# Optimization experiments

Measured on AMD Instinct MI355X. Metric: run time of the kernel, lower is better.

The kernel has to match this reference:

```python
import jax, jax.numpy as jnp
import numpy as np


def _attention(v, W, static_hidden, dec_hidden):
    # static_hidden: [B,N,H], dec_hidden: [B,1,H], v: [1,1,H], W: [1,H,2H]
    hidden = jnp.concatenate(
        [static_hidden, jnp.broadcast_to(dec_hidden, static_hidden.shape)], axis=2
    )  # [B,N,2H]
    e = jnp.tanh(jnp.einsum('bnk,hk->bnh', hidden, W[0]))  # W @ hidden^T, done row-wise
    scores = jnp.einsum('bnh,h->bn', e, v[0, 0])  # [B,N]
    return jax.nn.softmax(scores, axis=1)[:, None, :]  # [B,1,N]


def _gru_step(x, h, w_ih, w_hh, b_ih, b_hh):
    # x: [B,H] input, h: [B,H] prev hidden; PyTorch gate order: r | z | n
    gx = x @ w_ih.T + b_ih  # [B,3H]
    gh = h @ w_hh.T + b_hh  # [B,3H]
    H = h.shape[-1]
    r = jax.nn.sigmoid(gx[:, :H] + gh[:, :H])
    z = jax.nn.sigmoid(gx[:, H:2 * H] + gh[:, H:2 * H])
    n = jnp.tanh(gx[:, 2 * H:] + r * gh[:, 2 * H:])
    return (1.0 - z) * n + z * h


def _pointer_scores(v, W, static_hidden, context, state_embedding):
    # energy = cat(static, context, state_emb) -> [B,N,3H]
    energy = jnp.concatenate(
        [static_hidden,
         jnp.broadcast_to(context, static_hidden.shape),
         jnp.broadcast_to(state_embedding, static_hidden.shape)], axis=2)
    e = jnp.tanh(jnp.einsum('bnk,hk->bnh', energy, W[0]))  # [B,N,H]
    return jnp.einsum('bnh,h->bn', e, v[0, 0])  # [B,N]


def setup_inputs() -> dict:
    key = jax.random.key(0)
    B, N, H = 128, 512, 512
    ks = jax.random.split(key, 16)
    s = 0.05
    return {
        'static_hidden': jax.random.normal(ks[0], (B, N, H), jnp.float32),
        'state_embedding': jax.random.normal(ks[1], (B, 1, H), jnp.float32),
        'decoder_hidden': jax.random.normal(ks[2], (B, 1, H), jnp.float32),
        'target_hidden': jax.random.normal(ks[3], (B, 1, H), jnp.float32),
        'last_hh': jax.random.normal(ks[4], (1, B, H), jnp.float32),
        # Pointer params (note: target branch of the original reuses self.v/self.W)
        'ptr_v': jax.random.normal(ks[5], (1, 1, H), jnp.float32) * s,
        'ptr_W': jax.random.normal(ks[6], (1, H, 3 * H), jnp.float32) * s,
        # encoder attention params
        'enc_v': jax.random.normal(ks[7], (1, 1, H), jnp.float32) * s,
        'enc_W': jax.random.normal(ks[8], (1, H, 2 * H), jnp.float32) * s,
        # target attention params
        'tgt_v': jax.random.normal(ks[9], (1, 1, H), jnp.float32) * s,
        'tgt_W': jax.random.normal(ks[10], (1, H, 2 * H), jnp.float32) * s,
        # GRU (single layer) params
        'gru_w_ih': jax.random.normal(ks[11], (3 * H, H), jnp.float32) * s,
        'gru_w_hh': jax.random.normal(ks[12], (3 * H, H), jnp.float32) * s,
        'gru_b_ih': jax.random.normal(ks[13], (3 * H,), jnp.float32) * s,
        'gru_b_hh': jax.random.normal(ks[14], (3 * H,), jnp.float32) * s,
    }


def reference(static_hidden, state_embedding, decoder_hidden, target_hidden, last_hh,
              ptr_v, ptr_W, enc_v, enc_W, tgt_v, tgt_W,
              gru_w_ih, gru_w_hh, gru_b_ih, gru_b_hh):
    # GRU over seq len 1 (batch_first); dropout layers are identity (eval mode)
    h_new = _gru_step(decoder_hidden[:, 0, :], last_hh[0], gru_w_ih, gru_w_hh, gru_b_ih, gru_b_hh)
    rnn_out = h_new[:, None, :]          # [B,1,H]
    new_last_hh = h_new[None]            # [1,B,H]

    # encoder attention + context
    enc_attn = _attention(enc_v, enc_W, static_hidden, rnn_out)   # [B,1,N]
    context = jnp.matmul(enc_attn, static_hidden)                 # [B,1,H]
    probs = _pointer_scores(ptr_v, ptr_W, static_hidden, context, state_embedding)

    # target attention + context (original reuses self.v/self.W for scoring)
    tgt_attn = _attention(tgt_v, tgt_W, static_hidden, target_hidden)
    context_t = jnp.matmul(tgt_attn, static_hidden)
    probs_target = _pointer_scores(ptr_v, ptr_W, static_hidden, context_t, state_embedding)

    probs = 5.0 * probs + probs_target
    return (probs, new_last_hh)
```

## Files before the change

### kernel.cpp

```cpp
#include <hip/hip_runtime.h>
#include <math.h>

#define B 128
#define N 512
#define H 512

typedef __attribute__((ext_vector_type(8))) short short8;
typedef __attribute__((ext_vector_type(4))) float floatx4;

__device__ __forceinline__ float sigmoidf_(float x){ return 1.0f/(1.0f+__expf(-x)); }

__device__ __forceinline__ float fast_tanh(float x){
    float t = __expf(-2.0f*fabsf(x));
    float r = __fdividef(1.0f - t, 1.0f + t);
    return copysignf(r, x);
}

__device__ __forceinline__ unsigned f2bf1(float f){
    unsigned u = __float_as_uint(f);
    u += 0x7FFFu + ((u>>16)&1u);
    return u>>16;
}
__device__ __forceinline__ unsigned pk2(float a, float b){
    return f2bf1(a) | (f2bf1(b)<<16);
}

__global__ __launch_bounds__(256) void k_castA(const float* __restrict__ A,
    unsigned short* __restrict__ Abf)
{
    size_t i = ((size_t)blockIdx.x*256 + threadIdx.x)*8;
    float4 lo = *(const float4*)&A[i];
    float4 hi = *(const float4*)&A[i+4];
    uint4 p;
    p.x = pk2(lo.x,lo.y); p.y = pk2(lo.z,lo.w);
    p.z = pk2(hi.x,hi.y); p.w = pk2(hi.z,hi.w);
    *(uint4*)&Abf[i] = p;
}

__global__ __launch_bounds__(256) void k_castw(
    const float* __restrict__ encW, const float* __restrict__ tgtW,
    const float* __restrict__ ptrW, const float* __restrict__ wih,
    const float* __restrict__ whh,
    unsigned short* __restrict__ We_s, unsigned short* __restrict__ Wt_s,
    unsigned short* __restrict__ Wp_s, unsigned short* __restrict__ We_d,
    unsigned short* __restrict__ Wt_d, unsigned short* __restrict__ Wp_c,
    unsigned short* __restrict__ Wp_e, unsigned short* __restrict__ Wih_b,
    unsigned short* __restrict__ Whh_b)
{
    int r = blockIdx.x, t = threadIdx.x;
    const float* src; unsigned short* dst; int pitch, off, row;
    if (r < 512)      { src=encW; dst=We_s; pitch=2*H; off=0;   row=r; }
    else if (r<1024)  { src=tgtW; dst=Wt_s; pitch=2*H; off=0;   row=r-512; }
    else if (r<1536)  { src=ptrW; dst=Wp_s; pitch=3*H; off=0;   row=r-1024; }
    else if (r<2048)  { src=encW; dst=We_d; pitch=2*H; off=H;   row=r-1536; }
    else if (r<2560)  { src=tgtW; dst=Wt_d; pitch=2*H; off=H;   row=r-2048; }
    else if (r<3072)  { src=ptrW; dst=Wp_c; pitch=3*H; off=H;   row=r-2560; }
    else if (r<3584)  { src=ptrW; dst=Wp_e; pitch=3*H; off=2*H; row=r-3072; }
    else if (r<5120)  { src=wih;  dst=Wih_b;pitch=H;   off=0;   row=r-3584; }
    else              { src=whh;  dst=Whh_b;pitch=H;   off=0;   row=r-5120; }
    float2 v = *(const float2*)&src[(size_t)row*pitch + off + 2*t];
    *(unsigned*)&dst[(size_t)row*H + 2*t] = pk2(v.x, v.y);
}

__global__ __launch_bounds__(256) void k_castX(const float* __restrict__ dec,
    const float* __restrict__ lhh, const float* __restrict__ tgt,
    const float* __restrict__ sem,
    unsigned short* __restrict__ Xbf, unsigned short* __restrict__ Hbf,
    unsigned short* __restrict__ Tbf, unsigned short* __restrict__ Sbf)
{
    int blk = blockIdx.x; int mat = blk >> 5;
    const float* src = mat==0?dec : mat==1?lhh : mat==2?tgt : sem;
    unsigned short* dst = mat==0?Xbf : mat==1?Hbf : mat==2?Tbf : Sbf;
    size_t i = ((size_t)(blk&31)*256 + threadIdx.x)*8;
    float4 lo = *(const float4*)&src[i];
    float4 hi = *(const float4*)&src[i+4];
    uint4 p;
    p.x = pk2(lo.x,lo.y); p.y = pk2(lo.z,lo.w);
    p.z = pk2(hi.x,hi.y); p.w = pk2(hi.z,hi.w);
    *(uint4*)&dst[i] = p;
}

__global__ __launch_bounds__(256) void k_castctx(const float* __restrict__ ctx,
    const float* __restrict__ ctxt,
    unsigned short* __restrict__ CXbf, unsigned short* __restrict__ CTbf)
{
    int blk = blockIdx.x; int mat = blk >> 5;
    const float* src = mat ? ctxt : ctx;
    unsigned short* dst = mat ? CTbf : CXbf;
    size_t i = ((size_t)(blk&31)*256 + threadIdx.x)*8;
    float4 lo = *(const float4*)&src[i];
    float4 hi = *(const float4*)&src[i+4];
    uint4 p;
    p.x = pk2(lo.x,lo.y); p.y = pk2(lo.z,lo.w);
    p.z = pk2(hi.x,hi.y); p.w = pk2(hi.z,hi.w);
    *(uint4*)&dst[i] = p;
}

__device__ __forceinline__ void gemm128_tile(
    const unsigned short* __restrict__ Ab,
    const unsigned short* __restrict__ Bb,
    float* __restrict__ C, int ldc)
{
    __shared__ __align__(16) unsigned short As[128*64];
    __shared__ __align__(16) unsigned short Bs[128*64];
    int t = threadIdx.x;
    int lane = t & 63, wave = t >> 6;
    int wy = wave >> 1, wx = wave & 1;
    int li = lane & 15, quad = lane >> 4;

    floatx4 acc[4][4];
    #pragma unroll
    for (int i=0;i<4;++i)
      #pragma unroll
      for (int j=0;j<4;++j) acc[i][j] = (floatx4)(0.0f);

    for (int kt=0; kt<8; ++kt){
        int k0 = kt*64;
        #pragma unroll
        for (int c=0;c<4;++c){
            int idx = c*256 + t;
            int row = idx >> 3, kb = idx & 7;
            uint4 va = *(const uint4*)&Ab[(size_t)row*512 + k0 + kb*8];
            *(uint4*)&As[row*64 + ((kb ^ (row&7))*8)] = va;
            uint4 vb = *(const uint4*)&Bb[(size_t)row*512 + k0 + kb*8];
            *(uint4*)&Bs[row*64 + ((kb ^ (row&7))*8)] = vb;
        }
        __syncthreads();
        #pragma unroll
        for (int ks=0;ks<2;++ks){
            short8 af[4], bg[4];
            #pragma unroll
            for (int i=0;i<4;++i){
                int m = wy*64 + i*16 + li;
                int kb = (ks*4 + quad) ^ (m&7);
                af[i] = *(const short8*)&As[m*64 + kb*8];
            }
            #pragma unroll
            for (int j=0;j<4;++j){
                int h = wx*64 + j*16 + li;
                int kb = (ks*4 + quad) ^ (h&7);
                bg[j] = *(const short8*)&Bs[h*64 + kb*8];
            }
            #pragma unroll
            for (int i=0;i<4;++i)
              #pragma unroll
              for (int j=0;j<4;++j)
                acc[i][j] = __builtin_amdgcn_mfma_f32_16x16x32_bf16(af[i], bg[j], acc[i][j], 0,0,0);
        }
        __syncthreads();
    }
    #pragma unroll
    for (int i=0;i<4;++i)
      #pragma unroll
      for (int j=0;j<4;++j)
        #pragma unroll
        for (int rg=0;rg<4;++rg){
            int m = wy*64 + i*16 + quad*4 + rg;
            int n = wx*64 + j*16 + li;
            C[(size_t)m*ldc + n] = acc[i][j][rg];
        }
}

__global__ __launch_bounds__(256,2) void k_gru_gemm(
    const unsigned short* __restrict__ Xbf, const unsigned short* __restrict__ Hbf,
    const unsigned short* __restrict__ Wih_b, const unsigned short* __restrict__ Whh_b,
    float* __restrict__ gx, float* __restrict__ gh)
{
    int blk = blockIdx.x;
    int mat = blk / 12, nt = blk % 12;
    const unsigned short* Ab = mat ? Hbf : Xbf;
    const unsigned short* Bb = (mat ? Whh_b : Wih_b) + (size_t)nt*128*512;
    float* C = (mat ? gh : gx) + nt*128;
    gemm128_tile(Ab, Bb, C, 3*H);
}

__global__ __launch_bounds__(256) void k_gru_gate(const float* __restrict__ gx,
    const float* __restrict__ gh, const float* __restrict__ lhh,
    const float* __restrict__ bih, const float* __restrict__ bhh,
    float* __restrict__ out_hh, unsigned short* __restrict__ hnew_bf)
{
    int idx = blockIdx.x*256 + threadIdx.x;
    int b = idx >> 9, k = idx & 511;
    const float* gxb = gx + (size_t)b*(3*H);
    const float* ghb = gh + (size_t)b*(3*H);
    float r = sigmoidf_(gxb[k]     + bih[k]     + ghb[k]     + bhh[k]);
    float z = sigmoidf_(gxb[H+k]   + bih[H+k]   + ghb[H+k]   + bhh[H+k]);
    float n = tanhf(gxb[2*H+k] + bih[2*H+k] + r*(ghb[2*H+k] + bhh[2*H+k]));
    float h = (1.f-z)*n + z*lhh[idx];
    out_hh[idx] = h;
    hnew_bf[idx] = (unsigned short)f2bf1(h);
}

__global__ __launch_bounds__(256,2) void k_bias_gemm(
    const unsigned short* __restrict__ HNbf, const unsigned short* __restrict__ Tbf,
    const unsigned short* __restrict__ Sbf,
    const unsigned short* __restrict__ We_d, const unsigned short* __restrict__ Wt_d,
    const unsigned short* __restrict__ Wp_e,
    float* __restrict__ d_enc, float* __restrict__ d_tgt, float* __restrict__ d_se)
{
    int blk = blockIdx.x;
    int mat = blk >> 2, nt = blk & 3;
    const unsigned short* Ab = mat==0 ? HNbf : mat==1 ? Tbf : Sbf;
    const unsigned short* Bb = (mat==0 ? We_d : mat==1 ? Wt_d : Wp_e) + (size_t)nt*128*512;
    float* C = (mat==0 ? d_enc : mat==1 ? d_tgt : d_se) + nt*128;
    gemm128_tile(Ab, Bb, C, H);
}

__global__ __launch_bounds__(256,2) void k_dptr_gemm(
    const unsigned short* __restrict__ CXbf, const unsigned short* __restrict__ CTbf,
    const unsigned short* __restrict__ Wp_c,
    float* __restrict__ d_pe, float* __restrict__ d_pt)
{
    int blk = blockIdx.x;
    int mat = blk >> 2, nt = blk & 3;
    const unsigned short* Ab = mat ? CTbf : CXbf;
    const unsigned short* Bb = Wp_c + (size_t)nt*128*512;
    float* C = (mat ? d_pt : d_pe) + nt*128;
    gemm128_tile(Ab, Bb, C, H);
}

template<bool BF16A>
__global__ __launch_bounds__(256,2) void k_scores_fused(
    const float* __restrict__ Af, const unsigned short* __restrict__ Abf,
    const unsigned short* __restrict__ We, const unsigned short* __restrict__ Wt,
    const float* __restrict__ d_enc, const float* __restrict__ d_tgt,
    const float* __restrict__ enc_v, const float* __restrict__ tgt_v,
    float* __restrict__ sc_e, float* __restrict__ sc_t)
{
    __shared__ __align__(16) unsigned short As[128*64];
    __shared__ __align__(16) unsigned short Be[128*64];
    __shared__ __align__(16) unsigned short Bt[128*64];
    int blk = blockIdx.x;
    int b = blk >> 4; int nt = (blk >> 2) & 3; int ht = blk & 3;
    int n0 = nt*128, hb = ht*128;
    int t = threadIdx.x;
    int lane = t & 63, wave = t >> 6;
    int wy = wave >> 1, wx = wave & 1;
    int li = lane & 15, quad = lane >> 4;

    floatx4 acc_e[4][4], acc_t[4][4];
    #pragma unroll
    for (int i=0;i<4;++i)
      #pragma unroll
      for (int j=0;j<4;++j){ acc_e[i][j]=(floatx4)(0.0f); acc_t[i][j]=(floatx4)(0.0f); }

    for (int kt=0; kt<8; ++kt){
        int k0 = kt*64;
        #pragma unroll
        for (int c=0;c<4;++c){
            int idx = c*256 + t;
            int row = idx >> 3, kb = idx & 7;
            if constexpr (BF16A){
                uint4 v = *(const uint4*)&Abf[(size_t)(b*N+n0+row)*H + k0 + kb*8];
                *(uint4*)&As[row*64 + ((kb ^ (row&7))*8)] = v;
            } else {
                const float* src = Af + (size_t)(b*N+n0+row)*H + k0 + kb*8;
                float4 lo = *(const float4*)src;
                float4 hi = *(const float4*)(src+4);
                uint4 p;
                p.x = pk2(lo.x,lo.y); p.y = pk2(lo.z,lo.w);
                p.z = pk2(hi.x,hi.y); p.w = pk2(hi.z,hi.w);
                *(uint4*)&As[row*64 + ((kb ^ (row&7))*8)] = p;
            }
        }
        #pragma unroll
        for (int c=0;c<4;++c){
            int idx = c*256 + t;
            int row = idx >> 3, kb = idx & 7;
            uint4 v = *(const uint4*)&We[(size_t)(hb+row)*H + k0 + kb*8];
            *(uint4*)&Be[row*64 + ((kb ^ (row&7))*8)] = v;
            uint4 w = *(const uint4*)&Wt[(size_t)(hb+row)*H + k0 + kb*8];
            *(uint4*)&Bt[row*64 + ((kb ^ (row&7))*8)] = w;
        }
        __syncthreads();
        #pragma unroll
        for (int ks=0;ks<2;++ks){
            short8 af[4], be[4], bt[4];
            #pragma unroll
            for (int i=0;i<4;++i){
                int m = wy*64 + i*16 + li;
                int kb = (ks*4 + quad) ^ (m&7);
                af[i] = *(const short8*)&As[m*64 + kb*8];
            }
            #pragma unroll
            for (int j=0;j<4;++j){
                int h = wx*64 + j*16 + li;
                int kb = (ks*4 + quad) ^ (h&7);
                be[j] = *(const short8*)&Be[h*64 + kb*8];
                bt[j] = *(const short8*)&Bt[h*64 + kb*8];
            }
            #pragma unroll
            for (int i=0;i<4;++i)
              #pragma unroll
              for (int j=0;j<4;++j){
                acc_e[i][j] = __builtin_amdgcn_mfma_f32_16x16x32_bf16(af[i], be[j], acc_e[i][j], 0,0,0);
                acc_t[i][j] = __builtin_amdgcn_mfma_f32_16x16x32_bf16(af[i], bt[j], acc_t[i][j], 0,0,0);
              }
        }
        __syncthreads();
    }
    float nse[4][4], nst[4][4];
    #pragma unroll
    for (int i=0;i<4;++i)
      #pragma unroll
      for (int rg=0;rg<4;++rg){ nse[i][rg]=0.f; nst[i][rg]=0.f; }
    #pragma unroll
    for (int j=0;j<4;++j){
        int hm = hb + wx*64 + j*16 + li;
        float dje = d_enc[b*H+hm], vje = enc_v[hm];
        float djt = d_tgt[b*H+hm], vjt = tgt_v[hm];
        #pragma unroll
        for (int i=0;i<4;++i)
          #pragma unroll
          for (int rg=0;rg<4;++rg){
            nse[i][rg] += vje * fast_tanh(acc_e[i][j][rg] + dje);
            nst[i][rg] += vjt * fast_tanh(acc_t[i][j][rg] + djt);
          }
    }
    #pragma unroll
    for (int off=1; off<16; off<<=1)
      #pragma unroll
      for (int i=0;i<4;++i)
        #pragma unroll
        for (int rg=0;rg<4;++rg){
          nse[i][rg] += __shfl_xor(nse[i][rg], off);
          nst[i][rg] += __shfl_xor(nst[i][rg], off);
        }
    if (li==0){
        #pragma unroll
        for (int i=0;i<4;++i)
          #pragma unroll
          for (int rg=0;rg<4;++rg){
            atomicAdd(&sc_e[b*N + n0 + wy*64 + i*16 + quad*4 + rg], nse[i][rg]);
            atomicAdd(&sc_t[b*N + n0 + wy*64 + i*16 + quad*4 + rg], nst[i][rg]);
          }
    }
}

__global__ __launch_bounds__(256) void k_softmax(const float* __restrict__ sc_e,
    const float* __restrict__ sc_t, float* __restrict__ w_e, float* __restrict__ w_t)
{
    __shared__ float buf[256];
    int b = blockIdx.x, t = threadIdx.x;
    float x0 = sc_e[b*N+t], x1 = sc_e[b*N+t+256];
    float m = fmaxf(x0,x1);
    buf[t]=m; __syncthreads();
    for (int s2=128;s2>0;s2>>=1){ if(t<s2) buf[t]=fmaxf(buf[t],buf[t+s2]); __syncthreads(); }
    m = buf[0]; __syncthreads();
    float e0 = __expf(x0-m), e1 = __expf(x1-m);
    buf[t]=e0+e1; __syncthreads();
    for (int s2=128;s2>0;s2>>=1){ if(t<s2) buf[t]+=buf[t+s2]; __syncthreads(); }
    float inv = 1.0f/buf[0]; __syncthreads();
    w_e[b*N+t]=e0*inv; w_e[b*N+t+256]=e1*inv;
    x0 = sc_t[b*N+t]; x1 = sc_t[b*N+t+256];
    m = fmaxf(x0,x1);
    buf[t]=m; __syncthreads();
    for (int s2=128;s2>0;s2>>=1){ if(t<s2) buf[t]=fmaxf(buf[t],buf[t+s2]); __syncthreads(); }
    m = buf[0]; __syncthreads();
    e0 = __expf(x0-m); e1 = __expf(x1-m);
    buf[t]=e0+e1; __syncthreads();
    for (int s2=128;s2>0;s2>>=1){ if(t<s2) buf[t]+=buf[t+s2]; __syncthreads(); }
    inv = 1.0f/buf[0];
    w_t[b*N+t]=e0*inv; w_t[b*N+t+256]=e1*inv;
}

__global__ __launch_bounds__(256) void k_context_bf16(const unsigned short* __restrict__ Abf,
    const float* __restrict__ w_e, const float* __restrict__ w_t,
    float* __restrict__ ctx, float* __restrict__ ctxt)
{
    __shared__ float we[64], wt[64];
    int b = blockIdx.x >> 3, c = blockIdx.x & 7, t = threadIdx.x;
    int n0 = c*64;
    if (t < 64){ we[t]=w_e[b*N+n0+t]; wt[t]=w_t[b*N+n0+t]; }
    __syncthreads();
    float ae0=0.f, ae1=0.f, at0=0.f, at1=0.f;
    for (int n=0;n<64;++n){
        unsigned u = *(const unsigned*)&Abf[(size_t)(b*N+n0+n)*H + 2*t];
        float lo = __uint_as_float(u<<16);
        float hi = __uint_as_float(u & 0xFFFF0000u);
        float e = we[n], g = wt[n];
        ae0 += e*lo; ae1 += e*hi; at0 += g*lo; at1 += g*hi;
    }
    atomicAdd(&ctx[b*H+2*t],   ae0); atomicAdd(&ctx[b*H+2*t+1],  ae1);
    atomicAdd(&ctxt[b*H+2*t],  at0); atomicAdd(&ctxt[b*H+2*t+1], at1);
}

__global__ __launch_bounds__(256) void k_context(const float* __restrict__ A,
    const float* __restrict__ w_e, const float* __restrict__ w_t,
    float* __restrict__ ctx, float* __restrict__ ctxt)
{
    __shared__ float we[128], wt[128];
    int b = blockIdx.x >> 2, c = blockIdx.x & 3, t = threadIdx.x;
    int n0 = c*128;
    if (t < 128){ we[t]=w_e[b*N+n0+t]; wt[t]=w_t[b*N+n0+t]; }
    __syncthreads();
    float ae0=0.f, ae1=0.f, at0=0.f, at1=0.f;
    for (int n=0;n<128;++n){
        const float* ar = A + (size_t)(b*N + n0 + n)*H;
        float a0 = ar[t], a1 = ar[t+256];
        ae0 += we[n]*a0; ae1 += we[n]*a1;
        at0 += wt[n]*a0; at1 += wt[n]*a1;
    }
    atomicAdd(&ctx[b*H+t],      ae0); atomicAdd(&ctx[b*H+t+256],  ae1);
    atomicAdd(&ctxt[b*H+t],     at0); atomicAdd(&ctxt[b*H+t+256], at1);
}

template<bool BF16A>
__global__ __launch_bounds__(256) void k_probs_mfma(
    const float* __restrict__ Af, const unsigned short* __restrict__ Abf,
    const unsigned short* __restrict__ Wp,
    const float* __restrict__ d_pe, const float* __restrict__ d_pt,
    const float* __restrict__ d_se,
    const float* __restrict__ ptr_v, float* __restrict__ probs)
{
    __shared__ __align__(16) unsigned short As[128*64];
    __shared__ __align__(16) unsigned short Bs[128*64];
    int blk = blockIdx.x;
    int b = blk >> 4; int nt = (blk >> 2) & 3; int ht = blk & 3;
    int n0 = nt*128, hb = ht*128;

    int t = threadIdx.x;
    int lane = t & 63, wave = t >> 6;
    int wy = wave >> 1, wx = wave & 1;
    int li = lane & 15, quad = lane >> 4;

    floatx4 acc[4][4];
    #pragma unroll
    for (int i=0;i<4;++i)
      #pragma unroll
      for (int j=0;j<4;++j) acc[i][j] = (floatx4)(0.0f);

    for (int kt=0; kt<8; ++kt){
        int k0 = kt*64;
        #pragma unroll
        for (int c=0;c<4;++c){
            int idx = c*256 + t;
            int row = idx >> 3, kb = idx & 7;
            if constexpr (BF16A){
                uint4 v = *(const uint4*)&Abf[(size_t)(b*N+n0+row)*H + k0 + kb*8];
                *(uint4*)&As[row*64 + ((kb ^ (row&7))*8)] = v;
            } else {
                const float* src = Af + (size_t)(b*N+n0+row)*H + k0 + kb*8;
                float4 lo = *(const float4*)src;
                float4 hi = *(const float4*)(src+4);
                uint4 p;
                p.x = pk2(lo.x,lo.y); p.y = pk2(lo.z,lo.w);
                p.z = pk2(hi.x,hi.y); p.w = pk2(hi.z,hi.w);
                *(uint4*)&As[row*64 + ((kb ^ (row&7))*8)] = p;
            }
        }
        #pragma unroll
        for (int c=0;c<4;++c){
            int idx = c*256 + t;
            int row = idx >> 3, kb = idx & 7;
            uint4 v = *(const uint4*)&Wp[(size_t)(hb+row)*H + k0 + kb*8];
            *(uint4*)&Bs[row*64 + ((kb ^ (row&7))*8)] = v;
        }
        __syncthreads();
        #pragma unroll
        for (int ks=0;ks<2;++ks){
            short8 af[4], bg[4];
            #pragma unroll
            for (int i=0;i<4;++i){
                int m = wy*64 + i*16 + li;
                int kb = (ks*4 + quad) ^ (m&7);
                af[i] = *(const short8*)&As[m*64 + kb*8];
            }
            #pragma unroll
            for (int j=0;j<4;++j){
                int h = wx*64 + j*16 + li;
                int kb = (ks*4 + quad) ^ (h&7);
                bg[j] = *(const short8*)&Bs[h*64 + kb*8];
            }
            #pragma unroll
            for (int i=0;i<4;++i)
              #pragma unroll
              for (int j=0;j<4;++j)
                acc[i][j] = __builtin_amdgcn_mfma_f32_16x16x32_bf16(af[i], bg[j], acc[i][j], 0,0,0);
        }
        __syncthreads();
    }
    float nsum[4][4];
    #pragma unroll
    for (int i=0;i<4;++i){ nsum[i][0]=0.f;nsum[i][1]=0.f;nsum[i][2]=0.f;nsum[i][3]=0.f; }
    #pragma unroll
    for (int j=0;j<4;++j){
        int hm = hb + wx*64 + j*16 + li;
        float se = d_se[b*H + hm];
        float de = d_pe[b*H + hm] + se;
        float dt = d_pt[b*H + hm] + se;
        float vj = ptr_v[hm];
        #pragma unroll
        for (int i=0;i<4;++i)
          #pragma unroll
          for (int rg=0;rg<4;++rg){
            float s = acc[i][j][rg];
            nsum[i][rg] += vj * (5.0f*fast_tanh(s + de) + fast_tanh(s + dt));
          }
    }
    #pragma unroll
    for (int off=1; off<16; off<<=1)
      #pragma unroll
      for (int i=0;i<4;++i)
        #pragma unroll
        for (int rg=0;rg<4;++rg)
          nsum[i][rg] += __shfl_xor(nsum[i][rg], off);
    if (li==0){
        #pragma unroll
        for (int i=0;i<4;++i)
          #pragma unroll
          for (int rg=0;rg<4;++rg)
            atomicAdd(&probs[b*N + n0 + wy*64 + i*16 + quad*4 + rg], nsum[i][rg]);
    }
}

extern "C" void kernel_launch(void* const* d_in, const int* in_sizes, int n_in,
                              void* d_out, int out_size, void* d_ws, size_t ws_size,
                              hipStream_t stream)
{
    (void)in_sizes; (void)n_in; (void)out_size;
    const float* A    = (const float*)d_in[0];
    const float* sem  = (const float*)d_in[1];
    const float* dec  = (const float*)d_in[2];
    const float* tgt  = (const float*)d_in[3];
    const float* lhh  = (const float*)d_in[4];
    const float* ptrv = (const float*)d_in[5];
    const float* ptrW = (const float*)d_in[6];
    const float* encv = (const float*)d_in[7];
    const float* encW = (const float*)d_in[8];
    const float* tgtv = (const float*)d_in[9];
    const float* tgtW = (const float*)d_in[10];
    const float* wih  = (const float*)d_in[11];
    const float* whh  = (const float*)d_in[12];
    const float* bih  = (const float*)d_in[13];
    const float* bhh  = (const float*)d_in[14];

    float* probs_out = (float*)d_out;
    float* hh_out    = (float*)d_out + B*N;

    float* ws = (float*)d_ws;
    const size_t S = (size_t)B*H;
    float* d_enc = ws;
    float* d_tgt = ws + S;
    float* d_se  = ws + 2*S;
    float* sc_e  = ws + 3*S;
    float* sc_t  = ws + 4*S;
    float* ctx   = ws + 5*S;
    float* ctxt  = ws + 6*S;
    float* w_e   = ws + 7*S;
    float* w_t   = ws + 8*S;
    float* d_pe  = ws + 9*S;
    float* d_pt  = ws + 10*S;
    float* gx    = ws + 11*S;
    float* gh    = ws + 14*S;
    unsigned short* bfb  = (unsigned short*)(ws + 17*S);
    const size_t WH = (size_t)H*H;
    const size_t WG = (size_t)3*H*H;
    unsigned short* We_s  = bfb;
    unsigned short* Wt_s  = We_s + WH;
    unsigned short* Wp_s  = Wt_s + WH;
    unsigned short* We_d  = Wp_s + WH;
    unsigned short* Wt_d  = We_d + WH;
    unsigned short* Wp_c  = Wt_d + WH;
    unsigned short* Wp_e  = Wp_c + WH;
    unsigned short* Wih_b = Wp_e + WH;
    unsigned short* Whh_b = Wih_b + WG;
    unsigned short* Xbf   = Whh_b + WG;
    unsigned short* Hbf   = Xbf + S;
    unsigned short* Tbf   = Hbf + S;
    unsigned short* Sbf   = Tbf + S;
    unsigned short* HNbf  = Sbf + S;
    unsigned short* CXbf  = HNbf + S;
    unsigned short* CTbf  = CXbf + S;
    unsigned short* Abf   = CTbf + S;

    const size_t need_full = 17*S*sizeof(float)
        + (7*WH + 2*WG + 7*S + (size_t)B*N*H) * sizeof(unsigned short);
    const bool big = ws_size >= need_full;

    hipMemsetAsync(sc_e, 0, 4*S*sizeof(float), stream);
    hipMemsetAsync(probs_out, 0, (size_t)B*N*sizeof(float), stream);

    k_castw<<<6656, 256, 0, stream>>>(encW, tgtW, ptrW, wih, whh,
        We_s, Wt_s, Wp_s, We_d, Wt_d, Wp_c, Wp_e, Wih_b, Whh_b);
    k_castX<<<128, 256, 0, stream>>>(dec, lhh, tgt, sem, Xbf, Hbf, Tbf, Sbf);
    if (big) k_castA<<<(int)(((size_t)B*N*H)/(256*8)), 256, 0, stream>>>(A, Abf);

    k_gru_gemm<<<24, 256, 0, stream>>>(Xbf, Hbf, Wih_b, Whh_b, gx, gh);
    k_gru_gate<<<256, 256, 0, stream>>>(gx, gh, lhh, bih, bhh, hh_out, HNbf);
    k_bias_gemm<<<12, 256, 0, stream>>>(HNbf, Tbf, Sbf, We_d, Wt_d, Wp_e, d_enc, d_tgt, d_se);

    if (big)
        k_scores_fused<true ><<<2048, 256, 0, stream>>>(A, Abf, We_s, Wt_s, d_enc, d_tgt, encv, tgtv, sc_e, sc_t);
    else
        k_scores_fused<false><<<2048, 256, 0, stream>>>(A, Abf, We_s, Wt_s, d_enc, d_tgt, encv, tgtv, sc_e, sc_t);
    k_softmax<<<B, 256, 0, stream>>>(sc_e, sc_t, w_e, w_t);
    if (big)
        k_context_bf16<<<B*8, 256, 0, stream>>>(Abf, w_e, w_t, ctx, ctxt);
    else
        k_context<<<B*4, 256, 0, stream>>>(A, w_e, w_t, ctx, ctxt);

    k_castctx<<<64, 256, 0, stream>>>(ctx, ctxt, CXbf, CTbf);
    k_dptr_gemm<<<8, 256, 0, stream>>>(CXbf, CTbf, Wp_c, d_pe, d_pt);

    if (big)
        k_probs_mfma<true ><<<2048, 256, 0, stream>>>(A, Abf, Wp_s, d_pe, d_pt, d_se, ptrv, probs_out);
    else
        k_probs_mfma<false><<<2048, 256, 0, stream>>>(A, Abf, Wp_s, d_pe, d_pt, d_se, ptrv, probs_out);
}
```

Before: 504.3 us.

## Use direct global-to-LDS loads, merge cast kernels, fuse context cast into GEMM

```diff
diff --git a/kernel.cpp b/kernel.cpp
--- a/kernel.cpp
+++ b/kernel.cpp
@@ -7,6 +7,13 @@
 
 typedef __attribute__((ext_vector_type(8))) short short8;
 typedef __attribute__((ext_vector_type(4))) float floatx4;
+
+typedef const __attribute__((address_space(1))) unsigned int* gas_t;
+typedef __attribute__((address_space(3))) unsigned int* las_t;
+
+__device__ __forceinline__ void gl16(const void* g, void* l){
+    __builtin_amdgcn_global_load_lds((gas_t)g, (las_t)l, 16, 0, 0);
+}
 
 __device__ __forceinline__ float sigmoidf_(float x){ return 1.0f/(1.0f+__expf(-x)); }
 
@@ -25,75 +32,56 @@
     return f2bf1(a) | (f2bf1(b)<<16);
 }
 
-__global__ __launch_bounds__(256) void k_castA(const float* __restrict__ A,
-    unsigned short* __restrict__ Abf)
-{
-    size_t i = ((size_t)blockIdx.x*256 + threadIdx.x)*8;
-    float4 lo = *(const float4*)&A[i];
-    float4 hi = *(const float4*)&A[i+4];
-    uint4 p;
-    p.x = pk2(lo.x,lo.y); p.y = pk2(lo.z,lo.w);
-    p.z = pk2(hi.x,hi.y); p.w = pk2(hi.z,hi.w);
-    *(uint4*)&Abf[i] = p;
-}
-
-__global__ __launch_bounds__(256) void k_castw(
+__global__ __launch_bounds__(256) void k_cast_all(
     const float* __restrict__ encW, const float* __restrict__ tgtW,
     const float* __restrict__ ptrW, const float* __restrict__ wih,
     const float* __restrict__ whh,
+    const float* __restrict__ dec, const float* __restrict__ lhh,
+    const float* __restrict__ tgt, const float* __restrict__ sem,
+    const float* __restrict__ A,
     unsigned short* __restrict__ We_s, unsigned short* __restrict__ Wt_s,
     unsigned short* __restrict__ Wp_s, unsigned short* __restrict__ We_d,
     unsigned short* __restrict__ Wt_d, unsigned short* __restrict__ Wp_c,
     unsigned short* __restrict__ Wp_e, unsigned short* __restrict__ Wih_b,
-    unsigned short* __restrict__ Whh_b)
+    unsigned short* __restrict__ Whh_b,
+    unsigned short* __restrict__ Xbf, unsigned short* __restrict__ Hbf,
+    unsigned short* __restrict__ Tbf, unsigned short* __restrict__ Sbf,
+    unsigned short* __restrict__ Abf)
 {
     int r = blockIdx.x, t = threadIdx.x;
-    const float* src; unsigned short* dst; int pitch, off, row;
-    if (r < 512)      { src=encW; dst=We_s; pitch=2*H; off=0;   row=r; }
-    else if (r<1024)  { src=tgtW; dst=Wt_s; pitch=2*H; off=0;   row=r-512; }
-    else if (r<1536)  { src=ptrW; dst=Wp_s; pitch=3*H; off=0;   row=r-1024; }
-    else if (r<2048)  { src=encW; dst=We_d; pitch=2*H; off=H;   row=r-1536; }
-    else if (r<2560)  { src=tgtW; dst=Wt_d; pitch=2*H; off=H;   row=r-2048; }
-    else if (r<3072)  { src=ptrW; dst=Wp_c; pitch=3*H; off=H;   row=r-2560; }
-    else if (r<3584)  { src=ptrW; dst=Wp_e; pitch=3*H; off=2*H; row=r-3072; }
-    else if (r<5120)  { src=wih;  dst=Wih_b;pitch=H;   off=0;   row=r-3584; }
-    else              { src=whh;  dst=Whh_b;pitch=H;   off=0;   row=r-5120; }
-    float2 v = *(const float2*)&src[(size_t)row*pitch + off + 2*t];
-    *(unsigned*)&dst[(size_t)row*H + 2*t] = pk2(v.x, v.y);
-}
-
-__global__ __launch_bounds__(256) void k_castX(const float* __restrict__ dec,
-    const float* __restrict__ lhh, const float* __restrict__ tgt,
-    const float* __restrict__ sem,
-    unsigned short* __restrict__ Xbf, unsigned short* __restrict__ Hbf,
-    unsigned short* __restrict__ Tbf, unsigned short* __restrict__ Sbf)
-{
-    int blk = blockIdx.x; int mat = blk >> 5;
-    const float* src = mat==0?dec : mat==1?lhh : mat==2?tgt : sem;
-    unsigned short* dst = mat==0?Xbf : mat==1?Hbf : mat==2?Tbf : Sbf;
-    size_t i = ((size_t)(blk&31)*256 + threadIdx.x)*8;
-    float4 lo = *(const float4*)&src[i];
-    float4 hi = *(const float4*)&src[i+4];
-    uint4 p;
-    p.x = pk2(lo.x,lo.y); p.y = pk2(lo.z,lo.w);
-    p.z = pk2(hi.x,hi.y); p.w = pk2(hi.z,hi.w);
-    *(uint4*)&dst[i] = p;
-}
-
-__global__ __launch_bounds__(256) void k_castctx(const float* __restrict__ ctx,
-    const float* __restrict__ ctxt,
-    unsigned short* __restrict__ CXbf, unsigned short* __restrict__ CTbf)
-{
-    int blk = blockIdx.x; int mat = blk >> 5;
-    const float* src = mat ? ctxt : ctx;
-    unsigned short* dst = mat ? CTbf : CXbf;
-    size_t i = ((size_t)(blk&31)*256 + threadIdx.x)*8;
-    float4 lo = *(const float4*)&src[i];
-    float4 hi = *(const float4*)&src[i+4];
-    uint4 p;
-    p.x = pk2(lo.x,lo.y); p.y = pk2(lo.z,lo.w);
-    p.z = pk2(hi.x,hi.y); p.w = pk2(hi.z,hi.w);
-    *(uint4*)&dst[i] = p;
+    if (r < 6656){
+        const float* src; unsigned short* dst; int pitch, off, row;
+        if (r < 512)      { src=encW; dst=We_s; pitch=2*H; off=0;   row=r; }
+        else if (r<1024)  { src=tgtW; dst=Wt_s; pitch=2*H; off=0;   row=r-512; }
+        else if (r<1536)  { src=ptrW; dst=Wp_s; pitch=3*H; off=0;   row=r-1024; }
+        else if (r<2048)  { src=encW; dst=We_d; pitch=2*H; off=H;   row=r-1536; }
+        else if (r<2560)  { src=tgtW; dst=Wt_d; pitch=2*H; off=H;   row=r-2048; }
+        else if (r<3072)  { src=ptrW; dst=Wp_c; pitch=3*H; off=H;   row=r-2560; }
+        else if (r<3584)  { src=ptrW; dst=Wp_e; pitch=3*H; off=2*H; row=r-3072; }
+        else if (r<5120)  { src=wih;  dst=Wih_b;pitch=H;   off=0;   row=r-3584; }
+        else              { src=whh;  dst=Whh_b;pitch=H;   off=0;   row=r-5120; }
+        float2 v = *(const float2*)&src[(size_t)row*pitch + off + 2*t];
+        *(unsigned*)&dst[(size_t)row*H + 2*t] = pk2(v.x, v.y);
+    } else if (r < 6784){
+        int blk = r - 6656; int mat = blk >> 5;
+        const float* src = mat==0?dec : mat==1?lhh : mat==2?tgt : sem;
+        unsigned short* dst = mat==0?Xbf : mat==1?Hbf : mat==2?Tbf : Sbf;
+        size_t i = ((size_t)(blk&31)*256 + t)*8;
+        float4 lo = *(const float4*)&src[i];
+        float4 hi = *(const float4*)&src[i+4];
+        uint4 p;
+        p.x = pk2(lo.x,lo.y); p.y = pk2(lo.z,lo.w);
+        p.z = pk2(hi.x,hi.y); p.w = pk2(hi.z,hi.w);
+        *(uint4*)&dst[i] = p;
+    } else {
+        size_t i = ((size_t)(r-6784)*256 + t)*8;
+        float4 lo = *(const float4*)&A[i];
+        float4 hi = *(const float4*)&A[i+4];
+        uint4 p;
+        p.x = pk2(lo.x,lo.y); p.y = pk2(lo.z,lo.w);
+        p.z = pk2(hi.x,hi.y); p.w = pk2(hi.z,hi.w);
+        *(uint4*)&Abf[i] = p;
+    }
 }
 
 __device__ __forceinline__ void gemm128_tile(
@@ -118,12 +106,81 @@
         int k0 = kt*64;
         #pragma unroll
         for (int c=0;c<4;++c){
-            int idx = c*256 + t;
-            int row = idx >> 3, kb = idx & 7;
-            uint4 va = *(const uint4*)&Ab[(size_t)row*512 + k0 + kb*8];
-            *(uint4*)&As[row*64 + ((kb ^ (row&7))*8)] = va;
-            uint4 vb = *(const uint4*)&Bb[(size_t)row*512 + k0 + kb*8];
-            *(uint4*)&Bs[row*64 + ((kb ^ (row&7))*8)] = vb;
+            int s = c*256 + t;
+            int row = s >> 3;
+            int kb = (s & 7) ^ (row & 7);
+            gl16(&Ab[(size_t)row*512 + k0 + kb*8], &As[(size_t)s*8]);
+            gl16(&Bb[(size_t)row*512 + k0 + kb*8], &Bs[(size_t)s*8]);
+        }
+        __syncthreads();
+        #pragma unroll
+        for (int ks=0;ks<2;++ks){
+            short8 af[4], bg[4];
+            #pragma unroll
+            for (int i=0;i<4;++i){
+                int m = wy*64 + i*16 + li;
+                int kb = (ks*4 + quad) ^ (m&7);
+                af[i] = *(const short8*)&As[m*64 + kb*8];
+            }
+            #pragma unroll
+            for (int j=0;j<4;++j){
+                int h = wx*64 + j*16 + li;
+                int kb = (ks*4 + quad) ^ (h&7);
+                bg[j] = *(const short8*)&Bs[h*64 + kb*8];
+            }
+            #pragma unroll
+            for (int i=0;i<4;++i)
+              #pragma unroll
+              for (int j=0;j<4;++j)
+                acc[i][j] = __builtin_amdgcn_mfma_f32_16x16x32_bf16(af[i], bg[j], acc[i][j], 0,0,0);
+        }
+        __syncthreads();
+    }
+    #pragma unroll
+    for (int i=0;i<4;++i)
+      #pragma unroll
+      for (int j=0;j<4;++j)
+        #pragma unroll
+        for (int rg=0;rg<4;++rg){
+            int m = wy*64 + i*16 + quad*4 + rg;
+            int n = wx*64 + j*16 + li;
+            C[(size_t)m*ldc + n] = acc[i][j][rg];
+        }
+}
+
+__device__ __forceinline__ void gemm128_tile_f32A(
+    const float* __restrict__ Af,
+    const unsigned short* __restrict__ Bb,
+    float* __restrict__ C, int ldc)
+{
+    __shared__ __align__(16) unsigned short As[128*64];
+    __shared__ __align__(16) unsigned short Bs[128*64];
+    int t = threadIdx.x;
+    int lane = t & 63, wave = t >> 6;
+    int wy = wave >> 1, wx = wave & 1;
+    int li = lane & 15, quad = lane >> 4;
+
+    floatx4 acc[4][4];
+    #pragma unroll
+    for (int i=0;i<4;++i)
+      #pragma unroll
+      for (int j=0;j<4;++j) acc[i][j] = (floatx4)(0.0f);
+
+    for (int kt=0; kt<8; ++kt){
+        int k0 = kt*64;
+        #pragma unroll
+        for (int c=0;c<4;++c){
+            int s = c*256 + t;
+            int row = s >> 3;
+            int kb = (s & 7) ^ (row & 7);
+            gl16(&Bb[(size_t)row*512 + k0 + kb*8], &Bs[(size_t)s*8]);
+            const float* src = Af + (size_t)row*512 + k0 + kb*8;
+            float4 lo = *(const float4*)src;
+            float4 hi = *(const float4*)(src+4);
+            uint4 p;
+            p.x = pk2(lo.x,lo.y); p.y = pk2(lo.z,lo.w);
+            p.z = pk2(hi.x,hi.y); p.w = pk2(hi.z,hi.w);
+            *(uint4*)&As[(size_t)s*8] = p;
         }
         __syncthreads();
         #pragma unroll
@@ -207,16 +264,16 @@
 }
 
 __global__ __launch_bounds__(256,2) void k_dptr_gemm(
-    const unsigned short* __restrict__ CXbf, const unsigned short* __restrict__ CTbf,
+    const float* __restrict__ ctx, const float* __restrict__ ctxt,
     const unsigned short* __restrict__ Wp_c,
     float* __restrict__ d_pe, float* __restrict__ d_pt)
 {
     int blk = blockIdx.x;
     int mat = blk >> 2, nt = blk & 3;
-    const unsigned short* Ab = mat ? CTbf : CXbf;
+    const float* Af = mat ? ctxt : ctx;
     const unsigned short* Bb = Wp_c + (size_t)nt*128*512;
     float* C = (mat ? d_pt : d_pe) + nt*128;
-    gemm128_tile(Ab, Bb, C, H);
+    gemm128_tile_f32A(Af, Bb, C, H);
 }
 
 template<bool BF16A>
@@ -248,11 +305,11 @@
         int k0 = kt*64;
         #pragma unroll
         for (int c=0;c<4;++c){
-            int idx = c*256 + t;
-            int row = idx >> 3, kb = idx & 7;
+            int s = c*256 + t;
+            int row = s >> 3;
+            int kb = (s & 7) ^ (row & 7);
             if constexpr (BF16A){
-                uint4 v = *(const uint4*)&Abf[(size_t)(b*N+n0+row)*H + k0 + kb*8];
-                *(uint4*)&As[row*64 + ((kb ^ (row&7))*8)] = v;
+                gl16(&Abf[(size_t)(b*N+n0+row)*H + k0 + kb*8], &As[(size_t)s*8]);
             } else {
                 const float* src = Af + (size_t)(b*N+n0+row)*H + k0 + kb*8;
                 float4 lo = *(const float4*)src;
@@ -260,17 +317,10 @@
                 uint4 p;
                 p.x = pk2(lo.x,lo.y); p.y = pk2(lo.z,lo.w);
                 p.z = pk2(hi.x,hi.y); p.w = pk2(hi.z,hi.w);
-                *(uint4*)&As[row*64 + ((kb ^ (row&7))*8)] = p;
-            }
-        }
-        #pragma unroll
-        for (int c=0;c<4;++c){
-            int idx = c*256 + t;
-            int row = idx >> 3, kb = idx & 7;
-            uint4 v = *(const uint4*)&We[(size_t)(hb+row)*H + k0 + kb*8];
-            *(uint4*)&Be[row*64 + ((kb ^ (row&7))*8)] = v;
-            uint4 w = *(const uint4*)&Wt[(size_t)(hb+row)*H + k0 + kb*8];
-            *(uint4*)&Bt[row*64 + ((kb ^ (row&7))*8)] = w;
+                *(uint4*)&As[(size_t)s*8] = p;
+            }
+            gl16(&We[(size_t)(hb+row)*H + k0 + kb*8], &Be[(size_t)s*8]);
+            gl16(&Wt[(size_t)(hb+row)*H + k0 + kb*8], &Bt[(size_t)s*8]);
         }
         __syncthreads();
         #pragma unroll
@@ -406,7 +456,7 @@
 }
 
 template<bool BF16A>
-__global__ __launch_bounds__(256) void k_probs_mfma(
+__global__ __launch_bounds__(256,2) void k_probs_mfma(
     const float* __restrict__ Af, const unsigned short* __restrict__ Abf,
     const unsigned short* __restrict__ Wp,
     const float* __restrict__ d_pe, const float* __restrict__ d_pt,
@@ -434,11 +484,11 @@
         int k0 = kt*64;
         #pragma unroll
         for (int c=0;c<4;++c){
-            int idx = c*256 + t;
-            int row = idx >> 3, kb = idx & 7;
+            int s = c*256 + t;
+            int row = s >> 3;
+            int kb = (s & 7) ^ (row & 7);
             if constexpr (BF16A){
-                uint4 v = *(const uint4*)&Abf[(size_t)(b*N+n0+row)*H + k0 + kb*8];
-                *(uint4*)&As[row*64 + ((kb ^ (row&7))*8)] = v;
+                gl16(&Abf[(size_t)(b*N+n0+row)*H + k0 + kb*8], &As[(size_t)s*8]);
             } else {
                 const float* src = Af + (size_t)(b*N+n0+row)*H + k0 + kb*8;
                 float4 lo = *(const float4*)src;
@@ -446,15 +496,9 @@
                 uint4 p;
                 p.x = pk2(lo.x,lo.y); p.y = pk2(lo.z,lo.w);
                 p.z = pk2(hi.x,hi.y); p.w = pk2(hi.z,hi.w);
-                *(uint4*)&As[row*64 + ((kb ^ (row&7))*8)] = p;
-            }
-        }
-        #pragma unroll
-        for (int c=0;c<4;++c){
-            int idx = c*256 + t;
-            int row = idx >> 3, kb = idx & 7;
-            uint4 v = *(const uint4*)&Wp[(size_t)(hb+row)*H + k0 + kb*8];
-            *(uint4*)&Bs[row*64 + ((kb ^ (row&7))*8)] = v;
+                *(uint4*)&As[(size_t)s*8] = p;
+            }
+            gl16(&Wp[(size_t)(hb+row)*H + k0 + kb*8], &Bs[(size_t)s*8]);
         }
         __syncthreads();
         #pragma unroll
@@ -570,21 +614,20 @@
     unsigned short* Tbf   = Hbf + S;
     unsigned short* Sbf   = Tbf + S;
     unsigned short* HNbf  = Sbf + S;
-    unsigned short* CXbf  = HNbf + S;
-    unsigned short* CTbf  = CXbf + S;
-    unsigned short* Abf   = CTbf + S;
+    unsigned short* Abf   = HNbf + S;
 
     const size_t need_full = 17*S*sizeof(float)
-        + (7*WH + 2*WG + 7*S + (size_t)B*N*H) * sizeof(unsigned short);
+        + (7*WH + 2*WG + 5*S + (size_t)B*N*H) * sizeof(unsigned short);
     const bool big = ws_size >= need_full;
 
     hipMemsetAsync(sc_e, 0, 4*S*sizeof(float), stream);
     hipMemsetAsync(probs_out, 0, (size_t)B*N*sizeof(float), stream);
 
-    k_castw<<<6656, 256, 0, stream>>>(encW, tgtW, ptrW, wih, whh,
-        We_s, Wt_s, Wp_s, We_d, Wt_d, Wp_c, Wp_e, Wih_b, Whh_b);
-    k_castX<<<128, 256, 0, stream>>>(dec, lhh, tgt, sem, Xbf, Hbf, Tbf, Sbf);
-    if (big) k_castA<<<(int)(((size_t)B*N*H)/(256*8)), 256, 0, stream>>>(A, Abf);
+    int castA_blocks = big ? (int)(((size_t)B*N*H)/(256*8)) : 0;
+    k_cast_all<<<6784 + castA_blocks, 256, 0, stream>>>(encW, tgtW, ptrW, wih, whh,
+        dec, lhh, tgt, sem, A,
+        We_s, Wt_s, Wp_s, We_d, Wt_d, Wp_c, Wp_e, Wih_b, Whh_b,
+        Xbf, Hbf, Tbf, Sbf, Abf);
 
     k_gru_gemm<<<24, 256, 0, stream>>>(Xbf, Hbf, Wih_b, Whh_b, gx, gh);
     k_gru_gate<<<256, 256, 0, stream>>>(gx, gh, lhh, bih, bhh, hh_out, HNbf);
@@ -600,8 +643,7 @@
     else
         k_context<<<B*4, 256, 0, stream>>>(A, w_e, w_t, ctx, ctxt);
 
-    k_castctx<<<64, 256, 0, stream>>>(ctx, ctxt, CXbf, CTbf);
-    k_dptr_gemm<<<8, 256, 0, stream>>>(CXbf, CTbf, Wp_c, d_pe, d_pt);
+    k_dptr_gemm<<<8, 256, 0, stream>>>(ctx, ctxt, Wp_c, d_pe, d_pt);
 
     if (big)
         k_probs_mfma<true ><<<2048, 256, 0, stream>>>(A, Abf, Wp_s, d_pe, d_pt, d_se, ptrv, probs_out);
```

Measured after the change: 472.9 us. 6.2% less time.
